# Performance work log

Measured on AMD Instinct MI355X. Metric: run time of the kernel, lower is better.

The kernel has to match this reference:

```python
import jax, jax.numpy as jnp
import numpy as np
from jax import lax

NX, NY, NT = 24, 24, 10
NTYPE = 4
KS, KT = 20, 10
NNEURONS = [144, 144, 144, 144]
BATCH = 512


def _build_mask():
    # Faithful replication of the FixedLinear W construction. W is diagonal 0/1,
    # so F.linear(x, W) == x * diag(W); we only need the diagonal vector.
    np.random.seed(0)
    in_dim = NX * NY * NT * NTYPE
    d = np.zeros(in_dim, np.float32)
    for typ in range(NTYPE):
        density = np.sqrt(NX * NY / float(NNEURONS[typ]))
        totalcount = 0
        ycount = typ
        for y in range(NY):
            if ycount % density - density < -1:
                ycount += 1
            else:
                ycount += 1
                xcount = 0
                for x in range(NX):
                    if xcount % density >= 1:
                        xcount += 1
                    else:
                        xcount += 1
                        totalcount += 1
                        for t in range(NT):
                            idx = typ + NTYPE * t + NTYPE * NT * (NX * y + x)
                            d[idx] = 1.0
        leftover = NNEURONS[typ] - totalcount
        if leftover > 0:
            Px = np.random.permutation(NX * NY)
            for x_ in range(leftover):
                for t in range(NT):
                    idx = typ + NTYPE * t + NTYPE * NT * Px[x_]
                    d[idx] = 1.0
    return d


def setup_inputs() -> dict:
    key = jax.random.key(0)
    k1, k2, k3 = jax.random.split(key, 3)
    x = jax.random.normal(k1, (BATCH, NX, NY, NT, 1), jnp.float32)
    # conv weights (torch Conv3d layout OIDHW), no bias
    w1 = jax.random.normal(k2, (NTYPE, 1, KT, KS, KS), jnp.float32) * 0.05
    w2 = jax.random.normal(k3, (1, NTYPE, KT, KS, KS), jnp.float32) * 0.05
    # diagonal of FixedLinear W, reshaped to the (C,T,Y,X) activation layout
    mask = jnp.asarray(_build_mask()).reshape(NTYPE, NT, NY, NX)
    return {"x": x, "w1": w1, "w2": w2, "mask": mask}


def reference(x, w1, w2, mask):
    dn = ("NCDHW", "OIDHW", "NCDHW")
    # (B, X, Y, T, 1) -> (B, 1, T, Y, X)
    h = jnp.transpose(x, (0, 4, 3, 2, 1))
    # pad1 (D:(7,2), H:(19,19), W:(19,19)) fused into conv1; dilation (1,2,2)
    h = lax.conv_general_dilated(h, w1, window_strides=(1, 1, 1),
                                 padding=[(7, 2), (19, 19), (19, 19)],
                                 rhs_dilation=(1, 2, 2), dimension_numbers=dn)
    h = jax.nn.relu(h)                     # (B, NTYPE, NT, NY, NX)
    # FixedLinear with diagonal 0/1 W == elementwise mask multiply
    h = h * mask[None]
    # GaussianNoise: eval mode -> identity
    # pad2 (D:(7,2), H:(10,9), W:(10,9)) fused into conv2
    h = lax.conv_general_dilated(h, w2, window_strides=(1, 1, 1),
                                 padding=[(7, 2), (10, 9), (10, 9)],
                                 dimension_numbers=dn)
    # (B, 1, T, Y, X) -> (B, X, Y, T, 1)
    return jnp.transpose(h, (0, 4, 3, 2, 1))
```

## Files before the change

### kernel.cpp

```cpp
#include <hip/hip_runtime.h>


#define NSLOT 5760
static constexpr int P     = 10 * 24 * 24 * 512;
static constexpr int FBASE = 20480;
static constexpr int WZN   = 4 * 20 * 10 * 10 * 28;
static constexpr int W1SN  = 2 * 4 * 20 * 4 * 128 * 32;
static constexpr int XBT   = 24 * 4 * 512 * 32;

using bf16x8 = __attribute__((ext_vector_type(8))) short;
using f32x4  = __attribute__((ext_vector_type(4))) float;

__device__ __forceinline__ unsigned short f2bf(float f) {
  unsigned u = __float_as_uint(f);
  u += 0x7fff + ((u >> 16) & 1);
  return (unsigned short)(u >> 16);
}
__device__ __forceinline__ float bf2f(unsigned short h) {
  return __uint_as_float((unsigned)h << 16);
}

__device__ __forceinline__ void gload16(const void* g, void* l) {
  __builtin_amdgcn_global_load_lds(
      (const __attribute__((address_space(1))) unsigned int*)g,
      (__attribute__((address_space(3))) unsigned int*)l, 16, 0, 0);
}

__global__ __launch_bounds__(256) void k_xbt(const float* __restrict__ x,
                                             unsigned short* __restrict__ xbh,
                                             unsigned short* __restrict__ xbl) {
  __shared__ float lds[64][241];
  const int ix = blockIdx.x;
  const int b0 = blockIdx.y * 64;
  const int tid = threadIdx.x;
  const int p = ix & 1;
  const int c0 = (ix >> 1) * 10;
  #pragma unroll 4
  for (int i = 0; i < 60; ++i) {
    int idx = i * 256 + tid;
    int yt = idx % 240, lb = idx / 240;
    lds[lb][yt] = x[(size_t)(b0 + lb) * 5760 + ix * 240 + yt];
  }
  __syncthreads();
  #pragma unroll
  for (int i = 0; i < 6; ++i) {
    int q = i * 256 + tid;
    int lb = q & 63, y = q >> 6;
    const int b = b0 + lb;
    const float* src = &lds[lb][y * 10];
    #pragma unroll
    for (int k0 = 0; k0 < 10; ++k0) {
      const int k = c0 + k0;
      const int ks = k >> 5, kk = k & 31;
      const size_t a = (size_t)p * XBT +
                       (((size_t)(y * 4 + ks) * 512 + b) * 32 + kk);
      float f = src[k0];
      unsigned short hh = f2bf(f);
      xbh[a] = hh;
      xbl[a] = f2bf(f - bf2f(hh));
    }
    if (ix < 2) {
      #pragma unroll
      for (int k = 120; k < 128; ++k) {
        const size_t a = (size_t)p * XBT +
                         (((size_t)(y * 4 + 3) * 512 + b) * 32 + (k & 31));
        xbh[a] = 0; xbl[a] = 0;
      }
    }
  }
}

__global__ __launch_bounds__(256) void k_meta(const float* __restrict__ mask,
                                              int* __restrict__ bitmap,
                                              int* __restrict__ off,
                                              int* __restrict__ basep,
                                              int* __restrict__ cellmeta,
                                              float* __restrict__ mval) {
  __shared__ int tot[4];
  __shared__ int sb[4];
  const int tid = threadIdx.x;
  const int typ = tid >> 6, lane = tid & 63;
  int running = 0;
  for (int c = 0; c < 9; ++c) {
    const int pos = c * 64 + lane;
    int mb = 0;
    #pragma unroll
    for (int t = 0; t < 10; ++t)
      if (mask[typ * 5760 + t * 576 + pos] != 0.0f) mb |= (1 << t);
    bitmap[typ * 576 + pos] = mb;
    const int cnt = __popc(mb);
    int s = cnt;
    #pragma unroll
    for (int o = 1; o < 64; o <<= 1) {
      int v = __shfl_up(s, o, 64);
      if (lane >= o) s += v;
    }
    off[typ * 576 + pos] = running + s - cnt;
    running += __shfl(s, 63, 64);
  }
  if (lane == 63) tot[typ] = running;
  __syncthreads();
  if (tid == 0) {
    int a = 0;
    for (int q = 0; q < 4; ++q) { basep[q] = a; sb[q] = a; a += tot[q]; }
  }
  __syncthreads();
  for (int c = 0; c < 9; ++c) {
    const int pos = c * 64 + lane;
    const int mb = bitmap[typ * 576 + pos];
    int o = sb[typ] + off[typ * 576 + pos];
    const int ex = pos % 24;
    #pragma unroll
    for (int tp = 0; tp < 10; ++tp)
      if ((mb >> tp) & 1) {
        cellmeta[o] = tp * 280 + ex;
        mval[o] = mask[typ * 5760 + tp * 576 + pos];
        ++o;
      }
  }
}

__global__ __launch_bounds__(256) void k_wz(const float* __restrict__ w2,
                                            float* __restrict__ wz) {
  int idx = blockIdx.x * 256 + threadIdx.x;
  if (idx >= WZN) return;
  int c = idx % 28; int r = idx / 28;
  int ot = r % 10; r /= 10;
  int tp = r % 10; r /= 10;
  int ky = r % 20; int typ = r / 20;
  int kt = tp - ot + 7;
  float v = 0.0f;
  if (kt >= 0 && kt < 10 && c >= 3 && c <= 22)
    v = w2[typ * 4000 + kt * 400 + ky * 20 + (c - 3)];
  wz[idx] = v;
}

__global__ __launch_bounds__(256) void k_w1m(const float* __restrict__ w1,
                                             unsigned short* __restrict__ w1mh,
                                             unsigned short* __restrict__ w1ml) {
  int idx = blockIdx.x * 256 + threadIdx.x;
  if (idx >= W1SN) return;
  int kk = idx & 31;
  int r = (idx >> 5) & 127;
  int rest = idx >> 12;
  int ks = rest & 3; rest >>= 2;
  int ky = rest % 20; rest /= 20;
  int typ = rest % 4; int h = rest / 4;
  int c = ks * 32 + kk;
  float v = 0.0f;
  if (r < 120 && c < 120) {
    int ox = 2 * (r / 10) + (h == 0 ? 1 : 0);
    int ot = r % 10;
    int xx = 2 * (c / 10) + (h == 0 ? 0 : 1);
    int t  = c % 10;
    int sx = xx - ox + 19;
    int kt = t - ot + 7;
    if (sx >= 0 && sx <= 38 && (unsigned)kt <= 9u)
      v = w1[typ * 4000 + kt * 400 + ky * 20 + (sx >> 1)];
  }
  unsigned short h16 = f2bf(v);
  w1mh[idx] = h16;
  w1ml[idx] = f2bf(v - bf2f(h16));
}

__global__ __launch_bounds__(256) void k_conv1m(
    const unsigned short* __restrict__ xbh,
    const unsigned short* __restrict__ xbl,
    const unsigned short* __restrict__ w1mh,
    const unsigned short* __restrict__ w1ml,
    const int* __restrict__ bitmap, const int* __restrict__ off,
    const int* __restrict__ basep, const float* __restrict__ mval,
    float* __restrict__ h1c) {
  __shared__ unsigned short lds[2][12288];
  const int lin = blockIdx.x;
  const int cx = lin & 7;
  const int typ = cx >> 1, half = cx & 1;
  const int i = lin >> 3;
  const int n0 = (i & 7) * 64;
  const int rest = i >> 3;
  const int h = rest & 1;
  const int oy = half * 12 + (rest >> 1);
  const int w = threadIdx.x >> 6;
  const int lane = threadIdx.x & 63;
  const int l15 = lane & 15;
  const int kg = (lane >> 4) * 8;

  const int py = (oy + 1) & 1;
  int ylo = oy - 19; if (ylo < 0) ylo = 0;
  ylo += (ylo & 1) ^ py;
  int yhi = oy + 19; if (yhi > 23) yhi = 23;
  yhi -= (yhi & 1) ^ py;
  const int ns = (((yhi - ylo) >> 1) + 1) * 4;

  f32x4 acc[2][4];
  #pragma unroll
  for (int mi = 0; mi < 2; ++mi)
    #pragma unroll
    for (int nt = 0; nt < 4; ++nt) {
      f32x4 z = {0.f, 0.f, 0.f, 0.f};
      acc[mi][nt] = z;
    }

  auto stage = [&](int s, int bufi) {
    const int yy = ylo + ((s >> 2) << 1);
    const int ks = s & 3;
    const int ky = (yy - oy + 19) >> 1;
    const size_t asl = ((size_t)((h * 4 + typ) * 20 + ky) * 4 + ks) << 12;
    const unsigned short* Ah = w1mh + asl;
    const unsigned short* Al = w1ml + asl;
    const size_t bsl = (((size_t)(h * 24 + yy) * 4 + ks) << 14) +
                       (size_t)n0 * 32;
    const unsigned short* Bh = xbh + bsl;
    const unsigned short* Bl = xbl + bsl;
    char* lb = (char*)&lds[bufi][0];
    #pragma unroll
    for (int ia = 0; ia < 2; ++ia) {
      const int L = ia * 4096 + w * 1024 + lane * 16;
      const int row = L >> 6;
      const int g = row * 64 + ((((L >> 4) & 3) ^ ((row >> 1) & 3)) << 4);
      gload16((const char*)Ah + g, lb + ia * 4096 + w * 1024);
      gload16((const char*)Al + g, lb + 8192 + ia * 4096 + w * 1024);
    }
    {
      const int L = w * 1024 + lane * 16;
      const int row = L >> 6;
      const int g = row * 64 + ((((L >> 4) & 3) ^ ((row >> 1) & 3)) << 4);
      gload16((const char*)Bh + g, lb + 16384 + w * 1024);
      gload16((const char*)Bl + g, lb + 20480 + w * 1024);
    }
  };

  stage(0, 0);
  __syncthreads();
  int cur = 0;
  for (int s = 0; s < ns; ++s) {
    if (s + 1 < ns) stage(s + 1, cur ^ 1);
    const unsigned short* bufb = &lds[cur][0];
    bf16x8 bhv[4], blv[4];
    #pragma unroll
    for (int nt = 0; nt < 4; ++nt) {
      const int n = nt * 16 + l15;
      const int by = n * 64 + (((kg >> 3) ^ ((n >> 1) & 3)) << 4);
      bhv[nt] = *(const bf16x8*)((const char*)(bufb + 8192) + by);
      blv[nt] = *(const bf16x8*)((const char*)(bufb + 10240) + by);
    }
    #pragma unroll
    for (int mi = 0; mi < 2; ++mi) {
      const int r = (w * 2 + mi) * 16 + l15;
      const int ay = r * 64 + (((kg >> 3) ^ ((r >> 1) & 3)) << 4);
      const bf16x8 ah = *(const bf16x8*)((const char*)bufb + ay);
      const bf16x8 al = *(const bf16x8*)((const char*)(bufb + 4096) + ay);
      #pragma unroll
      for (int nt = 0; nt < 4; ++nt) {
        acc[mi][nt] = __builtin_amdgcn_mfma_f32_16x16x32_bf16(
            al, blv[nt], acc[mi][nt], 0, 0, 0);
        acc[mi][nt] = __builtin_amdgcn_mfma_f32_16x16x32_bf16(
            ah, blv[nt], acc[mi][nt], 0, 0, 0);
        acc[mi][nt] = __builtin_amdgcn_mfma_f32_16x16x32_bf16(
            al, bhv[nt], acc[mi][nt], 0, 0, 0);
        acc[mi][nt] = __builtin_amdgcn_mfma_f32_16x16x32_bf16(
            ah, bhv[nt], acc[mi][nt], 0, 0, 0);
      }
    }
    __syncthreads();
    cur ^= 1;
  }

  const int bo = basep[typ];
  #pragma unroll
  for (int mi = 0; mi < 2; ++mi) {
    #pragma unroll
    for (int reg = 0; reg < 4; ++reg) {
      const int r = (w * 2 + mi) * 16 + (lane >> 4) * 4 + reg;
      if (r >= 120) continue;
      const int ox = 2 * (r / 10) + (h == 0 ? 1 : 0);
      const int ot = r % 10;
      const int pos = oy * 24 + ox;
      const int mb = bitmap[typ * 576 + pos];
      if ((mb >> ot) & 1) {
        const int slot = bo + off[typ * 576 + pos] +
                         __popc(mb & ((1 << ot) - 1));
        const float mv = mval[slot];
        #pragma unroll
        for (int nt = 0; nt < 4; ++nt)
          h1c[(size_t)slot * 512 + n0 + nt * 16 + l15] =
              fmaxf(acc[mi][nt][reg], 0.0f) * mv;
      }
    }
  }
}

__global__ __launch_bounds__(256) void k_conv2(const float* __restrict__ h1c,
                                               const float* __restrict__ wz,
                                               const int* __restrict__ bitmap,
                                               const int* __restrict__ off,
                                               const int* __restrict__ basep,
                                               const int* __restrict__ cellmeta,
                                               float* __restrict__ part) {
  const int lin = blockIdx.x;
  const int cx = lin & 7, i = lin >> 3;
  const int typ = cx >> 1;
  const int oy  = (cx & 1) * 12 + (i % 12);
  const int x12 = i / 12;
  const int tile = x12 >> 1, bh = x12 & 1;
  const int ox0 = tile * 4;
  const int b = bh * 256 + threadIdx.x;
  const int bo = __builtin_amdgcn_readfirstlane(basep[typ]);

  float acc[40];
  #pragma unroll
  for (int i2 = 0; i2 < 40; ++i2) acc[i2] = 0.0f;

  const int ex_lo = ox0 - 10 < 0 ? 0 : ox0 - 10;
  const int ex_hi = ox0 + 12 > 23 ? 23 : ox0 + 12;
  const int ey0 = oy - 10 < 0 ? 0 : oy - 10;
  const int ey1 = oy + 9 > 23 ? 23 : oy + 9;

  for (int ey = ey0; ey <= ey1; ++ey) {
    const int ky = ey - oy + 10;
    const int rowb = typ * 576 + ey * 24;
    const int s_lo = bo + __builtin_amdgcn_readfirstlane(off[rowb + ex_lo]);
    const int s_hi = bo + __builtin_amdgcn_readfirstlane(off[rowb + ex_hi]) +
                     __popc(__builtin_amdgcn_readfirstlane(bitmap[rowb + ex_hi]));
    const int rbase = (typ * 20 + ky) * 2800 + 10 - ox0;
    int s = s_lo;
    for (; s + 2 <= s_hi; s += 2) {
      const int m0 = __builtin_amdgcn_readfirstlane(cellmeta[s]);
      const int m1 = __builtin_amdgcn_readfirstlane(cellmeta[s + 1]);
      const float xv0 = h1c[(size_t)s * 512 + b];
      const float xv1 = h1c[(size_t)(s + 1) * 512 + b];
      const float* wr0 = wz + rbase + m0;
      const float* wr1 = wz + rbase + m1;
      #pragma unroll
      for (int ot = 0; ot < 10; ++ot)
        #pragma unroll
        for (int j = 0; j < 4; ++j)
          acc[ot * 4 + j] = fmaf(wr0[ot * 28 + 3 - j], xv0, acc[ot * 4 + j]);
      #pragma unroll
      for (int ot = 0; ot < 10; ++ot)
        #pragma unroll
        for (int j = 0; j < 4; ++j)
          acc[ot * 4 + j] = fmaf(wr1[ot * 28 + 3 - j], xv1, acc[ot * 4 + j]);
    }
    if (s < s_hi) {
      const int meta = __builtin_amdgcn_readfirstlane(cellmeta[s]);
      const float xv = h1c[(size_t)s * 512 + b];
      const float* wrow = wz + rbase + meta;
      #pragma unroll
      for (int ot = 0; ot < 10; ++ot)
        #pragma unroll
        for (int j = 0; j < 4; ++j)
          acc[ot * 4 + j] = fmaf(wrow[ot * 28 + 3 - j], xv, acc[ot * 4 + j]);
    }
  }
  #pragma unroll
  for (int ot = 0; ot < 10; ++ot)
    #pragma unroll
    for (int j = 0; j < 4; ++j)
      part[(size_t)(((typ * 10 + ot) * 24 + oy) * 24 + ox0 + j) * 512 + b] =
          acc[ot * 4 + j];
}

__global__ __launch_bounds__(256) void k_reduce(const float* __restrict__ part,
                                                float* __restrict__ out) {
  __shared__ float lds[64][241];
  const int xb = blockIdx.x;
  const int b0 = blockIdx.y * 64;
  const int tid = threadIdx.x;
  #pragma unroll 4
  for (int i = 0; i < 60; ++i) {
    int idx = i * 256 + tid;
    int yt = idx >> 6, lb = idx & 63;
    int y = yt / 10, t = yt % 10;
    size_t a = (size_t)((t * 24 + y) * 24 + xb) * 512 + b0 + lb;
    lds[lb][yt] = part[a] + part[a + P] + part[a + 2 * (size_t)P] +
                  part[a + 3 * (size_t)P];
  }
  __syncthreads();
  #pragma unroll 4
  for (int i = 0; i < 60; ++i) {
    int idx = i * 256 + tid;
    int yt = idx % 240, lb = idx / 240;
    out[(size_t)(b0 + lb) * 5760 + xb * 240 + yt] = lds[lb][yt];
  }
}

extern "C" void kernel_launch(void* const* d_in, const int* in_sizes, int n_in,
                              void* d_out, int out_size, void* d_ws, size_t ws_size,
                              hipStream_t stream) {
  const float* x    = (const float*)d_in[0];
  const float* w1   = (const float*)d_in[1];
  const float* w2   = (const float*)d_in[2];
  const float* mask = (const float*)d_in[3];
  float* out = (float*)d_out;
  float* wsf = (float*)d_ws;

  int* bitmap   = (int*)d_ws;
  int* off      = bitmap + 2304;
  int* basep    = bitmap + 4608;
  int* cellmeta = bitmap + 5120;
  float* mval   = wsf + 14336;
  float* part = wsf + FBASE;
  unsigned short* xbh  = (unsigned short*)(wsf + FBASE);
  unsigned short* xbl  = (unsigned short*)(wsf + FBASE + 1572864);
  unsigned short* w1mh = (unsigned short*)(wsf + FBASE + 3145728);
  unsigned short* w1ml = (unsigned short*)(wsf + FBASE + 4456448);
  float* h1c = wsf + FBASE + (size_t)4 * P;
  float* wz  = wsf + FBASE + (size_t)5 * P;

  k_meta<<<1, 256, 0, stream>>>(mask, bitmap, off, basep, cellmeta, mval);
  k_wz<<<(WZN + 255) / 256, 256, 0, stream>>>(w2, wz);
  k_w1m<<<(W1SN + 255) / 256, 256, 0, stream>>>(w1, w1mh, w1ml);
  k_xbt<<<dim3(24, 8), 256, 0, stream>>>(x, xbh, xbl);
  k_conv1m<<<1536, 256, 0, stream>>>(xbh, xbl, w1mh, w1ml,
                                     bitmap, off, basep, mval, h1c);
  k_conv2<<<1152, 256, 0, stream>>>(h1c, wz, bitmap, off, basep,
                                    cellmeta, part);
  k_reduce<<<dim3(24, 8), 256, 0, stream>>>(part, out);
}
```

Baseline: 454.4 us.

## Bucket conv2 input cells by time tap in LDS and software-pipeline loads

k_conv2 now builds per-block lists in shared memory that group active compressed cells by their input time index. For each time tap it runs only the valid output-time range instead of all 10 output times, which skips FMAs against zero-padded weights. It also double-buffers the h1c and weight loads so the next cell's loads overlap the current cell's FMAs. The cost is a list-building prologue with LDS atomics, two barriers and more register pressure. Each bucket is also silently capped at 256 entries.

```diff
diff --git a/kernel.cpp b/kernel.cpp
--- a/kernel.cpp
+++ b/kernel.cpp
@@ -295,64 +295,103 @@
                                                const int* __restrict__ bitmap,
                                                const int* __restrict__ off,
                                                const int* __restrict__ basep,
-                                               const int* __restrict__ cellmeta,
                                                float* __restrict__ part) {
+  __shared__ int bcnt[10];
+  __shared__ int bls[10][256];
+  __shared__ int blw[10][256];
   const int lin = blockIdx.x;
-  const int cx = lin & 7, i = lin >> 3;
+  const int cx = lin & 7, i0 = lin >> 3;
   const int typ = cx >> 1;
-  const int oy  = (cx & 1) * 12 + (i % 12);
-  const int x12 = i / 12;
+  const int oy  = (cx & 1) * 12 + (i0 % 12);
+  const int x12 = i0 / 12;
   const int tile = x12 >> 1, bh = x12 & 1;
   const int ox0 = tile * 4;
   const int b = bh * 256 + threadIdx.x;
-  const int bo = __builtin_amdgcn_readfirstlane(basep[typ]);
-
-  float acc[40];
-  #pragma unroll
-  for (int i2 = 0; i2 < 40; ++i2) acc[i2] = 0.0f;
+  const int bo = basep[typ];
 
   const int ex_lo = ox0 - 10 < 0 ? 0 : ox0 - 10;
   const int ex_hi = ox0 + 12 > 23 ? 23 : ox0 + 12;
   const int ey0 = oy - 10 < 0 ? 0 : oy - 10;
   const int ey1 = oy + 9 > 23 ? 23 : oy + 9;
 
-  for (int ey = ey0; ey <= ey1; ++ey) {
-    const int ky = ey - oy + 10;
-    const int rowb = typ * 576 + ey * 24;
-    const int s_lo = bo + __builtin_amdgcn_readfirstlane(off[rowb + ex_lo]);
-    const int s_hi = bo + __builtin_amdgcn_readfirstlane(off[rowb + ex_hi]) +
-                     __popc(__builtin_amdgcn_readfirstlane(bitmap[rowb + ex_hi]));
-    const int rbase = (typ * 20 + ky) * 2800 + 10 - ox0;
-    int s = s_lo;
-    for (; s + 2 <= s_hi; s += 2) {
-      const int m0 = __builtin_amdgcn_readfirstlane(cellmeta[s]);
-      const int m1 = __builtin_amdgcn_readfirstlane(cellmeta[s + 1]);
-      const float xv0 = h1c[(size_t)s * 512 + b];
-      const float xv1 = h1c[(size_t)(s + 1) * 512 + b];
-      const float* wr0 = wz + rbase + m0;
-      const float* wr1 = wz + rbase + m1;
+  if (threadIdx.x < 10) bcnt[threadIdx.x] = 0;
+  __syncthreads();
+  {
+    const int nr = ey1 - ey0 + 1, nw = ex_hi - ex_lo + 1;
+    for (int c = threadIdx.x; c < nr * nw; c += 256) {
+      const int r = c / nw, e = c - r * nw;
+      const int ey = ey0 + r, ex = ex_lo + e;
+      const int rowb = typ * 576 + ey * 24;
+      const int mb = bitmap[rowb + ex];
+      if (mb) {
+        const int sbase = bo + off[rowb + ex];
+        const int wbase = (typ * 20 + (ey - oy + 10)) * 2800 + 10 - ox0 + ex;
+        int rk = 0;
+        #pragma unroll
+        for (int tp = 0; tp < 10; ++tp)
+          if ((mb >> tp) & 1) {
+            const int idx = atomicAdd(&bcnt[tp], 1);
+            if (idx < 256) {
+              bls[tp][idx] = sbase + rk;
+              blw[tp][idx] = wbase + tp * 280;
+            }
+            ++rk;
+          }
+      }
+    }
+  }
+  __syncthreads();
+
+  float acc[40];
+  #pragma unroll
+  for (int q = 0; q < 40; ++q) acc[q] = 0.0f;
+
+  #pragma unroll
+  for (int tp = 0; tp < 10; ++tp) {
+    const int olo = tp < 2 ? 0 : tp - 2;
+    const int ohi = tp > 2 ? 9 : tp + 7;
+    const int NW = ohi - olo + 1;
+    const int cnt = __builtin_amdgcn_readfirstlane(bcnt[tp]);
+    float xA = 0.f, xB = 0.f;
+    float qA[10][4], qB[10][4];
+    auto LD = [&](int e, float& xv, float (&q)[10][4]) {
+      const int s  = __builtin_amdgcn_readfirstlane(bls[tp][e]);
+      const int wv = __builtin_amdgcn_readfirstlane(blw[tp][e]);
+      xv = h1c[(size_t)s * 512 + b];
+      const float* wp = wz + wv;
       #pragma unroll
-      for (int ot = 0; ot < 10; ++ot)
-        #pragma unroll
-        for (int j = 0; j < 4; ++j)
-          acc[ot * 4 + j] = fmaf(wr0[ot * 28 + 3 - j], xv0, acc[ot * 4 + j]);
+      for (int qq = 0; qq < 10; ++qq)
+        if (qq < NW) {
+          q[qq][0] = wp[(olo + qq) * 28 + 0];
+          q[qq][1] = wp[(olo + qq) * 28 + 1];
+          q[qq][2] = wp[(olo + qq) * 28 + 2];
+          q[qq][3] = wp[(olo + qq) * 28 + 3];
+        }
+    };
+    auto FMAB = [&](float xv, const float (&q)[10][4]) {
       #pragma unroll
-      for (int ot = 0; ot < 10; ++ot)
-        #pragma unroll
-        for (int j = 0; j < 4; ++j)
-          acc[ot * 4 + j] = fmaf(wr1[ot * 28 + 3 - j], xv1, acc[ot * 4 + j]);
-    }
-    if (s < s_hi) {
-      const int meta = __builtin_amdgcn_readfirstlane(cellmeta[s]);
-      const float xv = h1c[(size_t)s * 512 + b];
-      const float* wrow = wz + rbase + meta;
-      #pragma unroll
-      for (int ot = 0; ot < 10; ++ot)
-        #pragma unroll
-        for (int j = 0; j < 4; ++j)
-          acc[ot * 4 + j] = fmaf(wrow[ot * 28 + 3 - j], xv, acc[ot * 4 + j]);
-    }
-  }
+      for (int qq = 0; qq < 10; ++qq)
+        if (qq < NW) {
+          const int ot = olo + qq;
+          acc[ot * 4 + 3] = fmaf(q[qq][0], xv, acc[ot * 4 + 3]);
+          acc[ot * 4 + 2] = fmaf(q[qq][1], xv, acc[ot * 4 + 2]);
+          acc[ot * 4 + 1] = fmaf(q[qq][2], xv, acc[ot * 4 + 1]);
+          acc[ot * 4 + 0] = fmaf(q[qq][3], xv, acc[ot * 4 + 0]);
+        }
+    };
+    if (cnt > 0) LD(0, xA, qA);
+    int e = 0;
+    while (e < cnt) {
+      if (e + 1 < cnt) LD(e + 1, xB, qB);
+      FMAB(xA, qA);
+      ++e;
+      if (e >= cnt) break;
+      if (e + 1 < cnt) LD(e + 1, xA, qA);
+      FMAB(xB, qB);
+      ++e;
+    }
+  }
+
   #pragma unroll
   for (int ot = 0; ot < 10; ++ot)
     #pragma unroll
@@ -414,7 +453,6 @@
   k_xbt<<<dim3(24, 8), 256, 0, stream>>>(x, xbh, xbl);
   k_conv1m<<<1536, 256, 0, stream>>>(xbh, xbl, w1mh, w1ml,
                                      bitmap, off, basep, mval, h1c);
-  k_conv2<<<1152, 256, 0, stream>>>(h1c, wz, bitmap, off, basep,
-                                    cellmeta, part);
+  k_conv2<<<1152, 256, 0, stream>>>(h1c, wz, bitmap, off, basep, part);
   k_reduce<<<dim3(24, 8), 256, 0, stream>>>(part, out);
 }
```

Result: slower. 516.5 us (+13.7%).

## Use rotated aligned weight copies for vector loads and skip zero time taps in conv2

Applied to the files above, without the earlier changes.

Builds four shifted copies of the zero-padded conv2 weight table so that each slot's weight row can be read with aligned 16-byte vector loads instead of scalar loads. It also skips output-time rows whose temporal tap is out of range (zero weights), and replaces the 2-way unroll with a software-pipelined loop that prefetches the next slot's meta and activation. The cost is a weight table four times larger to build and hold. The meta value is now loaded into a vector register through inline asm and then readfirstlane'd, which may add latency.

```diff
diff --git a/kernel.cpp b/kernel.cpp
--- a/kernel.cpp
+++ b/kernel.cpp
@@ -120,19 +120,23 @@
   }
 }
 
-__global__ __launch_bounds__(256) void k_wz(const float* __restrict__ w2,
-                                            float* __restrict__ wz) {
+__global__ __launch_bounds__(256) void k_wz4(const float* __restrict__ w2,
+                                             float* __restrict__ wz4) {
   int idx = blockIdx.x * 256 + threadIdx.x;
-  if (idx >= WZN) return;
-  int c = idx % 28; int r = idx / 28;
-  int ot = r % 10; r /= 10;
-  int tp = r % 10; r /= 10;
-  int ky = r % 20; int typ = r / 20;
-  int kt = tp - ot + 7;
+  if (idx >= 4 * WZN) return;
+  int rr = idx / WZN;
+  int src = idx - rr * WZN + rr;
   float v = 0.0f;
-  if (kt >= 0 && kt < 10 && c >= 3 && c <= 22)
-    v = w2[typ * 4000 + kt * 400 + ky * 20 + (c - 3)];
-  wz[idx] = v;
+  if (src < WZN) {
+    int c = src % 28; int r = src / 28;
+    int ot = r % 10; r /= 10;
+    int tp = r % 10; r /= 10;
+    int ky = r % 20; int typ = r / 20;
+    int kt = tp - ot + 7;
+    if (kt >= 0 && kt < 10 && c >= 3 && c <= 22)
+      v = w2[typ * 4000 + kt * 400 + ky * 20 + (c - 3)];
+  }
+  wz4[idx] = v;
 }
 
 __global__ __launch_bounds__(256) void k_w1m(const float* __restrict__ w1,
@@ -291,7 +295,7 @@
 }
 
 __global__ __launch_bounds__(256) void k_conv2(const float* __restrict__ h1c,
-                                               const float* __restrict__ wz,
+                                               const float* __restrict__ wz4,
                                                const int* __restrict__ bitmap,
                                                const int* __restrict__ off,
                                                const int* __restrict__ basep,
@@ -316,41 +320,48 @@
   const int ey0 = oy - 10 < 0 ? 0 : oy - 10;
   const int ey1 = oy + 9 > 23 ? 23 : oy + 9;
 
+  auto doslot = [&](int meta, float xv, int rbase0) {
+    const int offf = meta + (10 - ox0);
+    const int rot = offf & 3;
+    const f32x4* wrow = (const f32x4*)(wz4 + (size_t)rot * WZN + rbase0 +
+                                       (offf - rot));
+    const int tp = __builtin_amdgcn_readfirstlane(meta) / 280;
+    #pragma unroll
+    for (int ot = 0; ot < 10; ++ot) {
+      if (ot >= tp - 2 && ot <= tp + 7) {
+        const f32x4 wv = wrow[ot * 7];
+        acc[ot * 4 + 0] = fmaf(wv[3], xv, acc[ot * 4 + 0]);
+        acc[ot * 4 + 1] = fmaf(wv[2], xv, acc[ot * 4 + 1]);
+        acc[ot * 4 + 2] = fmaf(wv[1], xv, acc[ot * 4 + 2]);
+        acc[ot * 4 + 3] = fmaf(wv[0], xv, acc[ot * 4 + 3]);
+      }
+    }
+  };
+
   for (int ey = ey0; ey <= ey1; ++ey) {
     const int ky = ey - oy + 10;
     const int rowb = typ * 576 + ey * 24;
     const int s_lo = bo + __builtin_amdgcn_readfirstlane(off[rowb + ex_lo]);
     const int s_hi = bo + __builtin_amdgcn_readfirstlane(off[rowb + ex_hi]) +
                      __popc(__builtin_amdgcn_readfirstlane(bitmap[rowb + ex_hi]));
-    const int rbase = (typ * 20 + ky) * 2800 + 10 - ox0;
+    const int rbase0 = (typ * 20 + ky) * 2800;
     int s = s_lo;
-    for (; s + 2 <= s_hi; s += 2) {
-      const int m0 = __builtin_amdgcn_readfirstlane(cellmeta[s]);
-      const int m1 = __builtin_amdgcn_readfirstlane(cellmeta[s + 1]);
-      const float xv0 = h1c[(size_t)s * 512 + b];
-      const float xv1 = h1c[(size_t)(s + 1) * 512 + b];
-      const float* wr0 = wz + rbase + m0;
-      const float* wr1 = wz + rbase + m1;
-      #pragma unroll
-      for (int ot = 0; ot < 10; ++ot)
-        #pragma unroll
-        for (int j = 0; j < 4; ++j)
-          acc[ot * 4 + j] = fmaf(wr0[ot * 28 + 3 - j], xv0, acc[ot * 4 + j]);
-      #pragma unroll
-      for (int ot = 0; ot < 10; ++ot)
-        #pragma unroll
-        for (int j = 0; j < 4; ++j)
-          acc[ot * 4 + j] = fmaf(wr1[ot * 28 + 3 - j], xv1, acc[ot * 4 + j]);
-    }
+    int metaA = 0; float xvA = 0.0f;
     if (s < s_hi) {
-      const int meta = __builtin_amdgcn_readfirstlane(cellmeta[s]);
-      const float xv = h1c[(size_t)s * 512 + b];
-      const float* wrow = wz + rbase + meta;
-      #pragma unroll
-      for (int ot = 0; ot < 10; ++ot)
-        #pragma unroll
-        for (int j = 0; j < 4; ++j)
-          acc[ot * 4 + j] = fmaf(wrow[ot * 28 + 3 - j], xv, acc[ot * 4 + j]);
+      int sv; asm("v_mov_b32 %0, %1" : "=v"(sv) : "s"(s));
+      metaA = cellmeta[sv];
+      xvA = h1c[(size_t)sv * 512 + b];
+    }
+    while (s < s_hi) {
+      int metaB = 0; float xvB = 0.0f;
+      if (s + 1 < s_hi) {
+        int sv; asm("v_mov_b32 %0, %1" : "=v"(sv) : "s"(s + 1));
+        metaB = cellmeta[sv];
+        xvB = h1c[(size_t)sv * 512 + b];
+      }
+      doslot(metaA, xvA, rbase0);
+      metaA = metaB; xvA = xvB;
+      ++s;
     }
   }
   #pragma unroll
@@ -406,15 +417,15 @@
   unsigned short* w1mh = (unsigned short*)(wsf + FBASE + 3145728);
   unsigned short* w1ml = (unsigned short*)(wsf + FBASE + 4456448);
   float* h1c = wsf + FBASE + (size_t)4 * P;
-  float* wz  = wsf + FBASE + (size_t)5 * P;
+  float* wz4 = wsf + FBASE + (size_t)5 * P;
 
   k_meta<<<1, 256, 0, stream>>>(mask, bitmap, off, basep, cellmeta, mval);
-  k_wz<<<(WZN + 255) / 256, 256, 0, stream>>>(w2, wz);
+  k_wz4<<<(4 * WZN + 255) / 256, 256, 0, stream>>>(w2, wz4);
   k_w1m<<<(W1SN + 255) / 256, 256, 0, stream>>>(w1, w1mh, w1ml);
   k_xbt<<<dim3(24, 8), 256, 0, stream>>>(x, xbh, xbl);
   k_conv1m<<<1536, 256, 0, stream>>>(xbh, xbl, w1mh, w1ml,
                                      bitmap, off, basep, mval, h1c);
-  k_conv2<<<1152, 256, 0, stream>>>(h1c, wz, bitmap, off, basep,
+  k_conv2<<<1152, 256, 0, stream>>>(h1c, wz4, bitmap, off, basep,
                                     cellmeta, part);
   k_reduce<<<dim3(24, 8), 256, 0, stream>>>(part, out);
 }
```

Result: slower. 1.162 ms (+155.6%).

## Reorder compacted cells by time-plane and skip zero temporal taps in conv2

Applied to the files above, without the earlier changes.

The compacted active-cell list is reorganised from per-position ordering (all time planes of a cell together) to per (type, time-plane, row) ordering built with wave ballots. conv2 then loops over each time plane separately and only accumulates the output time steps whose temporal kernel tap is in range, skipping FMAs against weights that are known to be zero. conv1 also drops the low-times-low term of its split-bf16 MFMA product, removing a quarter of the MFMAs at a small cost in precision. The extra per-time-plane loop adds scalar metadata loads and branch structure in conv2.

```diff
diff --git a/kernel.cpp b/kernel.cpp
--- a/kernel.cpp
+++ b/kernel.cpp
@@ -71,53 +71,46 @@
 }
 
 __global__ __launch_bounds__(256) void k_meta(const float* __restrict__ mask,
-                                              int* __restrict__ bitmap,
-                                              int* __restrict__ off,
+                                              int* __restrict__ rowb2,
+                                              int* __restrict__ tpbm,
                                               int* __restrict__ basep,
                                               int* __restrict__ cellmeta,
                                               float* __restrict__ mval) {
   __shared__ int tot[4];
   __shared__ int sb[4];
-  const int tid = threadIdx.x;
-  const int typ = tid >> 6, lane = tid & 63;
+  const int typ = threadIdx.x >> 6, lane = threadIdx.x & 63;
   int running = 0;
-  for (int c = 0; c < 9; ++c) {
-    const int pos = c * 64 + lane;
-    int mb = 0;
-    #pragma unroll
-    for (int t = 0; t < 10; ++t)
-      if (mask[typ * 5760 + t * 576 + pos] != 0.0f) mb |= (1 << t);
-    bitmap[typ * 576 + pos] = mb;
-    const int cnt = __popc(mb);
-    int s = cnt;
-    #pragma unroll
-    for (int o = 1; o < 64; o <<= 1) {
-      int v = __shfl_up(s, o, 64);
-      if (lane >= o) s += v;
-    }
-    off[typ * 576 + pos] = running + s - cnt;
-    running += __shfl(s, 63, 64);
-  }
-  if (lane == 63) tot[typ] = running;
+  for (int tp = 0; tp < 10; ++tp)
+    for (int ey = 0; ey < 24; ++ey) {
+      int act = 0;
+      if (lane < 24)
+        act = (mask[typ * 5760 + tp * 576 + ey * 24 + lane] != 0.0f) ? 1 : 0;
+      const unsigned long long bl = __ballot(act);
+      const int m = (int)(bl & 0xFFFFFFull);
+      if (lane == 0) {
+        rowb2[(typ * 10 + tp) * 24 + ey] = running;
+        tpbm[(typ * 10 + tp) * 24 + ey] = m;
+      }
+      running += __popc(m);
+    }
+  if (lane == 0) tot[typ] = running;
   __syncthreads();
-  if (tid == 0) {
+  if (threadIdx.x == 0) {
     int a = 0;
     for (int q = 0; q < 4; ++q) { basep[q] = a; sb[q] = a; a += tot[q]; }
   }
   __syncthreads();
-  for (int c = 0; c < 9; ++c) {
-    const int pos = c * 64 + lane;
-    const int mb = bitmap[typ * 576 + pos];
-    int o = sb[typ] + off[typ * 576 + pos];
-    const int ex = pos % 24;
-    #pragma unroll
-    for (int tp = 0; tp < 10; ++tp)
-      if ((mb >> tp) & 1) {
-        cellmeta[o] = tp * 280 + ex;
-        mval[o] = mask[typ * 5760 + tp * 576 + pos];
-        ++o;
-      }
-  }
+  for (int tp = 0; tp < 10; ++tp)
+    for (int ey = 0; ey < 24; ++ey) {
+      const int ii = (typ * 10 + tp) * 24 + ey;
+      const int m = tpbm[ii];
+      const int base = sb[typ] + rowb2[ii];
+      if (lane < 24 && ((m >> lane) & 1)) {
+        const int idx = base + __popc(m & ((1 << lane) - 1));
+        cellmeta[idx] = lane;
+        mval[idx] = mask[typ * 5760 + tp * 576 + ey * 24 + lane];
+      }
+    }
 }
 
 __global__ __launch_bounds__(256) void k_wz(const float* __restrict__ w2,
@@ -168,7 +161,7 @@
     const unsigned short* __restrict__ xbl,
     const unsigned short* __restrict__ w1mh,
     const unsigned short* __restrict__ w1ml,
-    const int* __restrict__ bitmap, const int* __restrict__ off,
+    const int* __restrict__ rowb2, const int* __restrict__ tpbm,
     const int* __restrict__ basep, const float* __restrict__ mval,
     float* __restrict__ h1c) {
   __shared__ unsigned short lds[2][12288];
@@ -253,8 +246,6 @@
       #pragma unroll
       for (int nt = 0; nt < 4; ++nt) {
         acc[mi][nt] = __builtin_amdgcn_mfma_f32_16x16x32_bf16(
-            al, blv[nt], acc[mi][nt], 0, 0, 0);
-        acc[mi][nt] = __builtin_amdgcn_mfma_f32_16x16x32_bf16(
             ah, blv[nt], acc[mi][nt], 0, 0, 0);
         acc[mi][nt] = __builtin_amdgcn_mfma_f32_16x16x32_bf16(
             al, bhv[nt], acc[mi][nt], 0, 0, 0);
@@ -275,11 +266,10 @@
       if (r >= 120) continue;
       const int ox = 2 * (r / 10) + (h == 0 ? 1 : 0);
       const int ot = r % 10;
-      const int pos = oy * 24 + ox;
-      const int mb = bitmap[typ * 576 + pos];
-      if ((mb >> ot) & 1) {
-        const int slot = bo + off[typ * 576 + pos] +
-                         __popc(mb & ((1 << ot) - 1));
+      const int ii = (typ * 10 + ot) * 24 + oy;
+      const int bm = tpbm[ii];
+      if ((bm >> ox) & 1) {
+        const int slot = bo + rowb2[ii] + __popc(bm & ((1 << ox) - 1));
         const float mv = mval[slot];
         #pragma unroll
         for (int nt = 0; nt < 4; ++nt)
@@ -292,8 +282,8 @@
 
 __global__ __launch_bounds__(256) void k_conv2(const float* __restrict__ h1c,
                                                const float* __restrict__ wz,
-                                               const int* __restrict__ bitmap,
-                                               const int* __restrict__ off,
+                                               const int* __restrict__ rowb2,
+                                               const int* __restrict__ tpbm,
                                                const int* __restrict__ basep,
                                                const int* __restrict__ cellmeta,
                                                float* __restrict__ part) {
@@ -315,42 +305,47 @@
   const int ex_hi = ox0 + 12 > 23 ? 23 : ox0 + 12;
   const int ey0 = oy - 10 < 0 ? 0 : oy - 10;
   const int ey1 = oy + 9 > 23 ? 23 : oy + 9;
-
-  for (int ey = ey0; ey <= ey1; ++ey) {
-    const int ky = ey - oy + 10;
-    const int rowb = typ * 576 + ey * 24;
-    const int s_lo = bo + __builtin_amdgcn_readfirstlane(off[rowb + ex_lo]);
-    const int s_hi = bo + __builtin_amdgcn_readfirstlane(off[rowb + ex_hi]) +
-                     __popc(__builtin_amdgcn_readfirstlane(bitmap[rowb + ex_hi]));
-    const int rbase = (typ * 20 + ky) * 2800 + 10 - ox0;
-    int s = s_lo;
-    for (; s + 2 <= s_hi; s += 2) {
-      const int m0 = __builtin_amdgcn_readfirstlane(cellmeta[s]);
-      const int m1 = __builtin_amdgcn_readfirstlane(cellmeta[s + 1]);
-      const float xv0 = h1c[(size_t)s * 512 + b];
-      const float xv1 = h1c[(size_t)(s + 1) * 512 + b];
-      const float* wr0 = wz + rbase + m0;
-      const float* wr1 = wz + rbase + m1;
-      #pragma unroll
-      for (int ot = 0; ot < 10; ++ot)
-        #pragma unroll
-        for (int j = 0; j < 4; ++j)
-          acc[ot * 4 + j] = fmaf(wr0[ot * 28 + 3 - j], xv0, acc[ot * 4 + j]);
-      #pragma unroll
-      for (int ot = 0; ot < 10; ++ot)
-        #pragma unroll
-        for (int j = 0; j < 4; ++j)
-          acc[ot * 4 + j] = fmaf(wr1[ot * 28 + 3 - j], xv1, acc[ot * 4 + j]);
-    }
-    if (s < s_hi) {
-      const int meta = __builtin_amdgcn_readfirstlane(cellmeta[s]);
-      const float xv = h1c[(size_t)s * 512 + b];
-      const float* wrow = wz + rbase + meta;
-      #pragma unroll
-      for (int ot = 0; ot < 10; ++ot)
+  const int mlo = (1 << ex_lo) - 1;
+  const int mhi = (ex_hi >= 23) ? 0xFFFFFF : ((1 << (ex_hi + 1)) - 1);
+
+  auto fb = [&](int ex, float xv, int rb2, int olo, int ohi) {
+    const float* wrow = wz + rb2 + ex;
+    #pragma unroll
+    for (int ot = 0; ot < 10; ++ot)
+      if (ot >= olo && ot <= ohi) {
         #pragma unroll
         for (int j = 0; j < 4; ++j)
           acc[ot * 4 + j] = fmaf(wrow[ot * 28 + 3 - j], xv, acc[ot * 4 + j]);
+      }
+  };
+
+  for (int ey = ey0; ey <= ey1; ++ey) {
+    const int ky = ey - oy + 10;
+    const int rbase = (typ * 20 + ky) * 2800 + 10 - ox0;
+    #pragma unroll
+    for (int tp = 0; tp < 10; ++tp) {
+      const int olo = tp < 2 ? 0 : tp - 2;
+      const int ohi = tp > 2 ? 9 : tp + 7;
+      const int ii = (typ * 10 + tp) * 24 + ey;
+      const int bm = __builtin_amdgcn_readfirstlane(tpbm[ii]);
+      const int rb = __builtin_amdgcn_readfirstlane(rowb2[ii]);
+      const int s_lo = bo + rb + __popc(bm & mlo);
+      const int s_hi = bo + rb + __popc(bm & mhi);
+      const int rb2 = rbase + tp * 280;
+      int s = s_lo;
+      for (; s + 2 <= s_hi; s += 2) {
+        const int e0 = __builtin_amdgcn_readfirstlane(cellmeta[s]);
+        const int e1 = __builtin_amdgcn_readfirstlane(cellmeta[s + 1]);
+        const float xv0 = h1c[(size_t)s * 512 + b];
+        const float xv1 = h1c[(size_t)(s + 1) * 512 + b];
+        fb(e0, xv0, rb2, olo, ohi);
+        fb(e1, xv1, rb2, olo, ohi);
+      }
+      if (s < s_hi) {
+        const int e0 = __builtin_amdgcn_readfirstlane(cellmeta[s]);
+        const float xv0 = h1c[(size_t)s * 512 + b];
+        fb(e0, xv0, rb2, olo, ohi);
+      }
     }
   }
   #pragma unroll
@@ -395,10 +390,10 @@
   float* out = (float*)d_out;
   float* wsf = (float*)d_ws;
 
-  int* bitmap   = (int*)d_ws;
-  int* off      = bitmap + 2304;
-  int* basep    = bitmap + 4608;
-  int* cellmeta = bitmap + 5120;
+  int* rowb2    = (int*)d_ws;
+  int* tpbm     = rowb2 + 960;
+  int* basep    = rowb2 + 4608;
+  int* cellmeta = rowb2 + 5120;
   float* mval   = wsf + 14336;
   float* part = wsf + FBASE;
   unsigned short* xbh  = (unsigned short*)(wsf + FBASE);
@@ -408,13 +403,13 @@
   float* h1c = wsf + FBASE + (size_t)4 * P;
   float* wz  = wsf + FBASE + (size_t)5 * P;
 
-  k_meta<<<1, 256, 0, stream>>>(mask, bitmap, off, basep, cellmeta, mval);
+  k_meta<<<1, 256, 0, stream>>>(mask, rowb2, tpbm, basep, cellmeta, mval);
   k_wz<<<(WZN + 255) / 256, 256, 0, stream>>>(w2, wz);
   k_w1m<<<(W1SN + 255) / 256, 256, 0, stream>>>(w1, w1mh, w1ml);
   k_xbt<<<dim3(24, 8), 256, 0, stream>>>(x, xbh, xbl);
   k_conv1m<<<1536, 256, 0, stream>>>(xbh, xbl, w1mh, w1ml,
-                                     bitmap, off, basep, mval, h1c);
-  k_conv2<<<1152, 256, 0, stream>>>(h1c, wz, bitmap, off, basep,
+                                     rowb2, tpbm, basep, mval, h1c);
+  k_conv2<<<1152, 256, 0, stream>>>(h1c, wz, rowb2, tpbm, basep,
                                     cellmeta, part);
   k_reduce<<<dim3(24, 8), 256, 0, stream>>>(part, out);
 }
```

Result: slower. 491.2 us (+8.1%).
